# Kernel optimization log

Hardware: AMD Instinct MI355X
Metric: run time of the kernel (lower is better)

Reference implementation:

```python
import jax, jax.numpy as jnp
import numpy as np

LAMBDA = 1.0          # lambda_param
SIGMA = 1.0           # RBF bandwidth (sigkernel convention: exp(-||x-y||^2 / sigma))
DYADIC_ORDER = 2
F = 2 ** DYADIC_ORDER # dyadic refinement factor per time axis

B, M_POP, DIM, SEQ_LEN = 4, 16, 8, 65


def _rbf_gram(X, Y):
    # X: (m, L, d), Y: (n, L, d) -> static kernel Gram (m, n, L, L)
    sx = jnp.sum(X * X, -1)                       # (m, L)
    sy = jnp.sum(Y * Y, -1)                       # (n, L)
    inner = jnp.einsum('isd,jtd->ijst', X, Y)     # (m, n, L, L)
    d2 = sx[:, None, :, None] + sy[None, :, None, :] - 2.0 * inner
    return jnp.exp(-d2 / SIGMA)


def _increments(G):
    # double increment of the static Gram over time, then dyadic refinement
    inc = G[..., 1:, 1:] + G[..., :-1, :-1] - G[..., 1:, :-1] - G[..., :-1, 1:]
    inc = jnp.repeat(jnp.repeat(inc, F, axis=-2), F, axis=-1) / (F * F)
    return inc  # (..., S, S) with S = F*(L-1)


def _solve_pde(M):
    # Goursat PDE explicit finite-difference scheme (as in sigkernel):
    # K[i+1,j+1] = (K[i+1,j]+K[i,j+1])*(1 + m/2 + m^2/12) - K[i,j]*(1 - m^2/12)
    dtype = M.dtype
    S = M.shape[0]

    def row_step(prev_row, m_row):
        def cell(k_left, inp):
            k00, k01, m = inp
            a = 1.0 + 0.5 * m + m * m * (1.0 / 12.0)
            b = 1.0 - m * m * (1.0 / 12.0)
            k_new = (k_left + k01) * a - k00 * b
            return k_new, k_new
        _, tail = jax.lax.scan(cell, jnp.asarray(1.0, dtype),
                               (prev_row[:-1], prev_row[1:], m_row))
        new_row = jnp.concatenate([jnp.ones((1,), dtype), tail])
        return new_row, None

    row0 = jnp.ones((S + 1,), dtype)
    last_row, _ = jax.lax.scan(row_step, row0, M)
    return last_row[-1]


def _gram_sig(X, Y):
    # signature kernel Gram matrix: X (m,L,d), Y (n,L,d) -> (m,n)
    Minc = _increments(_rbf_gram(X, Y))
    return jax.vmap(jax.vmap(_solve_pde))(Minc)


def setup_inputs() -> dict:
    key = jax.random.key(0)
    k1, k2 = jax.random.split(key)
    generated_samples = jax.random.normal(k1, (B, M_POP, DIM, SEQ_LEN), dtype=jnp.float32)
    real_sample = jax.random.normal(k2, (B, DIM, SEQ_LEN), dtype=jnp.float32)
    return {"generated_samples": generated_samples, "real_sample": real_sample}


def reference(generated_samples, real_sample):
    # generated_samples: (B, m, dim, L); real_sample: (B, dim, L)
    gen = jnp.swapaxes(generated_samples, -1, -2)          # (B, m, L, d)
    real = jnp.swapaxes(real_sample, -1, -2)[:, None]      # (B, 1, L, d)
    m = gen.shape[1]
    K_XX = jax.vmap(_gram_sig)(gen, gen)                   # (B, m, m)
    K_XY = jax.vmap(_gram_sig)(gen, real)                  # (B, m, 1)
    self_sim = (jnp.sum(K_XX, axis=(-1, -2))
                - jnp.trace(K_XX, axis1=-2, axis2=-1)) / (m * (m - 1))
    cross_sim = jnp.mean(K_XY, axis=(-1, -2))
    return jnp.mean(LAMBDA / 2.0 * self_sim - cross_sim)
```

## Files before the change

kernel.cpp:

```cpp
#include <hip/hip_runtime.h>


#define SEQ   65
#define DIMS  8
#define MPOP  16
#define NBATCH 4
#define NPAIR_XX 120
#define NBLOCKS (NBATCH*(NPAIR_XX + MPOP))
#define MROW  194

__device__ __forceinline__ float wave_shr1(float x) {
    int xi = __builtin_bit_cast(int, x);
    int r  = __builtin_amdgcn_update_dpp(xi, xi, 0x138, 0xF, 0xF, false);
    return __builtin_bit_cast(float, r);
}
__device__ __forceinline__ float wave_shl1(float x) {
    int xi = __builtin_bit_cast(int, x);
    int r  = __builtin_amdgcn_update_dpp(xi, xi, 0x130, 0xF, 0xF, false);
    return __builtin_bit_cast(float, r);
}

__global__ __launch_bounds__(64, 1) void sigker_kernel(
    const float* __restrict__ gen,
    const float* __restrict__ realp,
    float* __restrict__ ws)
{
    __shared__ __align__(16) float YsF[SEQ * DIMS];
    __shared__ float R64[SEQ];
    __shared__ float YnL[SEQ];
    __shared__ __align__(16) float MmL[64 * MROW];

    const int tid = threadIdx.x;
    const int I   = tid;
    const bool lane0 = (I == 0);
    const int bid = blockIdx.x;

    {
        float4 z4 = make_float4(0.f, 0.f, 0.f, 0.f);
        float4* M4 = (float4*)MmL;
        #pragma unroll
        for (int k = 0; k < (64 * MROW) / 4 / 64; ++k)
            M4[k * 64 + tid] = z4;
        if (tid < 32) M4[48 * 64 + tid] = z4;
    }

    int b, ii, jj; bool cross;
    if (bid < NBATCH * NPAIR_XX) {
        b = bid / NPAIR_XX;
        int p = bid % NPAIR_XX;
        int i = 0, acc = 0;
        while (p >= acc + (MPOP - 1 - i)) { acc += (MPOP - 1 - i); ++i; }
        ii = i; jj = i + 1 + (p - acc); cross = false;
    } else {
        int t = bid - NBATCH * NPAIR_XX;
        b = t / MPOP; ii = t % MPOP; jj = 0; cross = true;
    }

    const float* Xg = gen + (size_t)(b * MPOP + ii) * (DIMS * SEQ);
    const float* Yg = cross ? (realp + (size_t)b * (DIMS * SEQ))
                            : (gen + (size_t)(b * MPOP + jj) * (DIMS * SEQ));

    for (int f = tid; f < SEQ * DIMS; f += 64) {
        int d = f / SEQ, s = f - d * SEQ;
        YsF[s * DIMS + d] = Yg[f];
    }
    float x0[DIMS], x64[DIMS];
    float xn0 = 0.f, xn64 = 0.f;
    #pragma unroll
    for (int d = 0; d < DIMS; ++d) {
        x0[d]  = Xg[d * SEQ + I];
        x64[d] = Xg[d * SEQ + 64];
        xn0  += x0[d]  * x0[d];
        xn64 += x64[d] * x64[d];
    }
    __syncthreads();

    for (int t = tid; t < SEQ; t += 64) {
        const float4* yv = (const float4*)&YsF[t * DIMS];
        float4 ya = yv[0], yb = yv[1];
        float yn  = ya.x*ya.x + ya.y*ya.y + ya.z*ya.z + ya.w*ya.w
                  + yb.x*yb.x + yb.y*yb.y + yb.z*yb.z + yb.w*yb.w;
        float dot = x64[0]*ya.x + x64[1]*ya.y + x64[2]*ya.z + x64[3]*ya.w
                  + x64[4]*yb.x + x64[5]*yb.y + x64[6]*yb.z + x64[7]*yb.w;
        YnL[t] = yn;
        R64[t] = __expf(2.f*dot - xn64 - yn);
    }
    __syncthreads();

    float* mrowW = &MmL[I * MROW + 64];
    float ep, enp;
    {
        const float4* yv = (const float4*)&YsF[0];
        float4 ya = yv[0], yb = yv[1];
        float dot = x0[0]*ya.x + x0[1]*ya.y + x0[2]*ya.z + x0[3]*ya.w
                  + x0[4]*yb.x + x0[5]*yb.y + x0[6]*yb.z + x0[7]*yb.w;
        float e  = __expf(2.f*dot - xn0 - YnL[0]);
        float en = wave_shl1(e);
        en = (I == 63) ? R64[0] : en;
        ep = e; enp = en;
    }
    #pragma unroll 4
    for (int t = 1; t < SEQ; ++t) {
        const float4* yv = (const float4*)&YsF[t * DIMS];
        float4 ya = yv[0], yb = yv[1];
        float dot = x0[0]*ya.x + x0[1]*ya.y + x0[2]*ya.z + x0[3]*ya.w
                  + x0[4]*yb.x + x0[5]*yb.y + x0[6]*yb.z + x0[7]*yb.w;
        float e  = __expf(2.f*dot - xn0 - YnL[t]);
        float en = wave_shl1(e);
        en = (I == 63) ? R64[t] : en;
        mrowW[t - 1] = ((en - enp) + (ep - e)) * (1.0f / 16.0f);
        ep = e; enp = en;
    }

    const float* mpde = &MmL[193 * I + 64];
    float l0 = 1.f, l1 = 1.f, l2 = 1.f, l3 = 1.f;
    float b0 = 1.f, b1 = 1.f, b2 = 1.f, b3 = 1.f;
    float cnext = 1.f;

#define STEP(MV) do {                                                   \
        float t0_ = wave_shr1(b0);                                      \
        float t1_ = wave_shr1(b1);                                      \
        float t2_ = wave_shr1(b2);                                      \
        float t3_ = wave_shr1(b3);                                      \
        if (lane0) { t0_ = 1.f; t1_ = 1.f; t2_ = 1.f; t3_ = 1.f; }      \
        float cc_ = cnext; cnext = t3_;                                 \
        float m_   = (MV);                                              \
        float q12_ = m_ * m_ * (1.0f / 12.0f);                          \
        float a_   = 1.0f + 0.5f * m_ + q12_;                           \
        float nb_  = q12_ - 1.0f;                                       \
        float u0_ = a_ * t0_ + nb_ * cc_;                               \
        float u1_ = a_ * t1_ + nb_ * t0_;                               \
        float u2_ = a_ * t2_ + nb_ * t1_;                               \
        float u3_ = a_ * t3_ + nb_ * t2_;                               \
        float q1_ = a_ * l0 + u0_;                                      \
        float q2_ = a_ * q1_ + u1_;                                     \
        float q3_ = a_ * q2_ + u2_;                                     \
        float q4_ = a_ * q3_ + u3_;                                     \
        u0_ = a_ * q1_ + nb_ * l0;  u1_ = a_ * q2_ + nb_ * q1_;         \
        u2_ = a_ * q3_ + nb_ * q2_; u3_ = a_ * q4_ + nb_ * q3_;         \
        float r1_ = a_ * l1 + u0_;                                      \
        float r2_ = a_ * r1_ + u1_;                                     \
        float r3_ = a_ * r2_ + u2_;                                     \
        float r4_ = a_ * r3_ + u3_;                                     \
        u0_ = a_ * r1_ + nb_ * l1;  u1_ = a_ * r2_ + nb_ * r1_;         \
        u2_ = a_ * r3_ + nb_ * r2_; u3_ = a_ * r4_ + nb_ * r3_;         \
        float s1_ = a_ * l2 + u0_;                                      \
        float s2_ = a_ * s1_ + u1_;                                     \
        float s3_ = a_ * s2_ + u2_;                                     \
        float s4_ = a_ * s3_ + u3_;                                     \
        u0_ = a_ * s1_ + nb_ * l2;  u1_ = a_ * s2_ + nb_ * s1_;         \
        u2_ = a_ * s3_ + nb_ * s2_; u3_ = a_ * s4_ + nb_ * s3_;         \
        float v1_ = a_ * l3 + u0_;                                      \
        float v2_ = a_ * v1_ + u1_;                                     \
        float v3_ = a_ * v2_ + u2_;                                     \
        float v4_ = a_ * v3_ + u3_;                                     \
        b0 = v1_; b1 = v2_; b2 = v3_; b3 = v4_;                         \
        l0 = q4_; l1 = r4_; l2 = s4_; l3 = v4_;                         \
    } while (0)

    float m0 = mpde[0], m1 = mpde[1], m2 = mpde[2], m3 = mpde[3];
    float m4 = mpde[4], m5 = mpde[5], m6 = mpde[6], m7 = mpde[7];

    for (int g = 0; g < 15; ++g) {
        const int nb_ = (g + 1) * 8;
        float n0 = mpde[nb_ + 0], n1 = mpde[nb_ + 1];
        float n2 = mpde[nb_ + 2], n3 = mpde[nb_ + 3];
        float n4 = mpde[nb_ + 4], n5 = mpde[nb_ + 5];
        float n6 = mpde[nb_ + 6], n7 = mpde[nb_ + 7];
        STEP(m0); STEP(m1); STEP(m2); STEP(m3);
        STEP(m4); STEP(m5); STEP(m6); STEP(m7);
        m0 = n0; m1 = n1; m2 = n2; m3 = n3;
        m4 = n4; m5 = n5; m6 = n6; m7 = n7;
    }
    STEP(m0); STEP(m1); STEP(m2); STEP(m3);
    STEP(m4); STEP(m5); STEP(m6);
#undef STEP

    if (tid == 63) {
        float w = cross ? (-1.0f / 32.0f) : (1.0f / 480.0f);
        ws[bid] = w * b3;
    }
}

__global__ __launch_bounds__(64, 1) void sigker_reduce(
    const float* __restrict__ ws, float* __restrict__ out)
{
    const int lane = threadIdx.x;
    float s = 0.f;
    for (int k = lane; k < NBLOCKS; k += 64) s += ws[k];
    #pragma unroll
    for (int off = 32; off >= 1; off >>= 1) s += __shfl_xor(s, off);
    if (lane == 0) out[0] = s;
}

extern "C" void kernel_launch(void* const* d_in, const int* in_sizes, int n_in,
                              void* d_out, int out_size, void* d_ws, size_t ws_size,
                              hipStream_t stream) {
    const float* gen   = (const float*)d_in[0];
    const float* realp = (const float*)d_in[1];
    if (n_in >= 2 && in_sizes[0] == NBATCH * DIMS * SEQ) {
        gen   = (const float*)d_in[1];
        realp = (const float*)d_in[0];
    }
    float* ws  = (float*)d_ws;
    float* out = (float*)d_out;
    sigker_kernel<<<NBLOCKS, 64, 0, stream>>>(gen, realp, ws);
    sigker_reduce<<<1, 64, 0, stream>>>(ws, out);
}
```

Baseline: 85.59 us.

## Fuse reduction via last-block atomic counter, shrink skewed LDS buffer, pack FMAs

Removes the separate reduction kernel by having the last block to finish (detected through an atomic counter and threadfence) sum the per-pair results. The launch now adds a memset for the counter. The skewed M buffer goes from a 194-stride zero-padded layout to a compact 66-stride row with clamped indexing, which drops the large LDS zero-fill and shrinks shared memory. The dot products and parts of the PDE update are rewritten with 2-wide float vectors to encourage packed FMA instructions.

New measurement: 91.72 us. 7.2% more time.

```diff
diff --git a/kernel.cpp b/kernel.cpp
--- a/kernel.cpp
+++ b/kernel.cpp
@@ -6,8 +6,11 @@
 #define MPOP  16
 #define NBATCH 4
 #define NPAIR_XX 120
-#define NBLOCKS (NBATCH*(NPAIR_XX + MPOP))
-#define MROW  194
+#define NPAIRS (NBATCH*(NPAIR_XX + MPOP))
+#define MST 66
+
+typedef float v2f __attribute__((ext_vector_type(2)));
+static __device__ __forceinline__ v2f mk2(float x, float y) { return (v2f){x, y}; }
 
 __device__ __forceinline__ float wave_shr1(float x) {
     int xi = __builtin_bit_cast(int, x);
@@ -19,30 +22,67 @@
     int r  = __builtin_amdgcn_update_dpp(xi, xi, 0x130, 0xF, 0xF, false);
     return __builtin_bit_cast(float, r);
 }
+__device__ __forceinline__ float ldm(const float* base, int idx) {
+    return base[idx < 0 ? 0 : idx];
+}
+
+struct PS { float l0,l1,l2,l3,b0,b1,b2,b3,cn; };
+
+__device__ __forceinline__ void pde_step(PS& s, float m, bool lane0) {
+    float t0 = wave_shr1(s.b0);  t0 = lane0 ? 1.f : t0;
+    float t1 = wave_shr1(s.b1);  t1 = lane0 ? 1.f : t1;
+    float t2 = wave_shr1(s.b2);  t2 = lane0 ? 1.f : t2;
+    float t3 = wave_shr1(s.b3);  t3 = lane0 ? 1.f : t3;
+    float c = s.cn; s.cn = t3;
+    float mm  = m * m;
+    float q12 = mm * (1.0f / 12.0f);
+    float a   = (1.0f + q12) + 0.5f * m;
+    float nb  = q12 - 1.0f;
+    v2f av = mk2(a, a), nv = mk2(nb, nb);
+    v2f u01 = av * mk2(t0, t1) + nv * mk2(c,  t0);
+    v2f u23 = av * mk2(t2, t3) + nv * mk2(t1, t2);
+    float q1 = a * s.l0 + u01.x;
+    float q2 = a * q1   + u01.y;
+    float q3 = a * q2   + u23.x;
+    float q4 = a * q3   + u23.y;
+    u01 = av * mk2(q1, q2) + nv * mk2(s.l0, q1);
+    u23 = av * mk2(q3, q4) + nv * mk2(q2,  q3);
+    float r1 = a * s.l1 + u01.x;
+    float r2 = a * r1   + u01.y;
+    float r3 = a * r2   + u23.x;
+    float r4 = a * r3   + u23.y;
+    u01 = av * mk2(r1, r2) + nv * mk2(s.l1, r1);
+    u23 = av * mk2(r3, r4) + nv * mk2(r2,  r3);
+    float w1 = a * s.l2 + u01.x;
+    float w2 = a * w1   + u01.y;
+    float w3 = a * w2   + u23.x;
+    float w4 = a * w3   + u23.y;
+    u01 = av * mk2(w1, w2) + nv * mk2(s.l2, w1);
+    u23 = av * mk2(w3, w4) + nv * mk2(w2,  w3);
+    float v1 = a * s.l3 + u01.x;
+    float v2 = a * v1   + u01.y;
+    float v3 = a * v2   + u23.x;
+    float v4 = a * v3   + u23.y;
+    s.b0=v1; s.b1=v2; s.b2=v3; s.b3=v4;
+    s.l0=q4; s.l1=r4; s.l2=w4; s.l3=v4;
+}
 
 __global__ __launch_bounds__(64, 1) void sigker_kernel(
     const float* __restrict__ gen,
     const float* __restrict__ realp,
-    float* __restrict__ ws)
+    float* __restrict__ ws,
+    unsigned* __restrict__ cnt,
+    float* __restrict__ out)
 {
     __shared__ __align__(16) float YsF[SEQ * DIMS];
+    __shared__ float YnL[SEQ];
     __shared__ float R64[SEQ];
-    __shared__ float YnL[SEQ];
-    __shared__ __align__(16) float MmL[64 * MROW];
+    __shared__ float MmL[64 * MST];
 
     const int tid = threadIdx.x;
     const int I   = tid;
     const bool lane0 = (I == 0);
     const int bid = blockIdx.x;
-
-    {
-        float4 z4 = make_float4(0.f, 0.f, 0.f, 0.f);
-        float4* M4 = (float4*)MmL;
-        #pragma unroll
-        for (int k = 0; k < (64 * MROW) / 4 / 64; ++k)
-            M4[k * 64 + tid] = z4;
-        if (tid < 32) M4[48 * 64 + tid] = z4;
-    }
 
     int b, ii, jj; bool cross;
     if (bid < NBATCH * NPAIR_XX) {
@@ -60,41 +100,54 @@
     const float* Yg = cross ? (realp + (size_t)b * (DIMS * SEQ))
                             : (gen + (size_t)(b * MPOP + jj) * (DIMS * SEQ));
 
+    MmL[MST * I] = 0.f;  MmL[MST * I + 65] = 0.f;
     for (int f = tid; f < SEQ * DIMS; f += 64) {
         int d = f / SEQ, s = f - d * SEQ;
         YsF[s * DIMS + d] = Yg[f];
     }
-    float x0[DIMS], x64[DIMS];
-    float xn0 = 0.f, xn64 = 0.f;
-    #pragma unroll
-    for (int d = 0; d < DIMS; ++d) {
-        x0[d]  = Xg[d * SEQ + I];
-        x64[d] = Xg[d * SEQ + 64];
-        xn0  += x0[d]  * x0[d];
-        xn64 += x64[d] * x64[d];
+    v2f x01, x23, x45, x67, z01, z23, z45, z67;
+    {
+        float xv[DIMS], zv[DIMS];
+        #pragma unroll
+        for (int d = 0; d < DIMS; ++d) {
+            xv[d] = Xg[d * SEQ + I];
+            zv[d] = Xg[d * SEQ + 64];
+        }
+        x01 = mk2(xv[0],xv[1]); x23 = mk2(xv[2],xv[3]);
+        x45 = mk2(xv[4],xv[5]); x67 = mk2(xv[6],xv[7]);
+        z01 = mk2(zv[0],zv[1]); z23 = mk2(zv[2],zv[3]);
+        z45 = mk2(zv[4],zv[5]); z67 = mk2(zv[6],zv[7]);
+    }
+    float xn0, xn64;
+    {
+        v2f sx = x01*x01 + x23*x23 + x45*x45 + x67*x67;
+        v2f sz = z01*z01 + z23*z23 + z45*z45 + z67*z67;
+        xn0 = sx.x + sx.y;  xn64 = sz.x + sz.y;
     }
     __syncthreads();
 
     for (int t = tid; t < SEQ; t += 64) {
         const float4* yv = (const float4*)&YsF[t * DIMS];
         float4 ya = yv[0], yb = yv[1];
-        float yn  = ya.x*ya.x + ya.y*ya.y + ya.z*ya.z + ya.w*ya.w
-                  + yb.x*yb.x + yb.y*yb.y + yb.z*yb.z + yb.w*yb.w;
-        float dot = x64[0]*ya.x + x64[1]*ya.y + x64[2]*ya.z + x64[3]*ya.w
-                  + x64[4]*yb.x + x64[5]*yb.y + x64[6]*yb.z + x64[7]*yb.w;
+        v2f y01 = mk2(ya.x,ya.y), y23 = mk2(ya.z,ya.w);
+        v2f y45 = mk2(yb.x,yb.y), y67 = mk2(yb.z,yb.w);
+        v2f sn = y01*y01 + y23*y23 + y45*y45 + y67*y67;
+        v2f sd = z01*y01 + z23*y23 + z45*y45 + z67*y67;
+        float yn  = sn.x + sn.y;
+        float dot = sd.x + sd.y;
         YnL[t] = yn;
         R64[t] = __expf(2.f*dot - xn64 - yn);
     }
     __syncthreads();
 
-    float* mrowW = &MmL[I * MROW + 64];
+    float* mrow = &MmL[MST * I];
     float ep, enp;
     {
         const float4* yv = (const float4*)&YsF[0];
         float4 ya = yv[0], yb = yv[1];
-        float dot = x0[0]*ya.x + x0[1]*ya.y + x0[2]*ya.z + x0[3]*ya.w
-                  + x0[4]*yb.x + x0[5]*yb.y + x0[6]*yb.z + x0[7]*yb.w;
-        float e  = __expf(2.f*dot - xn0 - YnL[0]);
+        v2f sd = x01*mk2(ya.x,ya.y) + x23*mk2(ya.z,ya.w)
+               + x45*mk2(yb.x,yb.y) + x67*mk2(yb.z,yb.w);
+        float e  = __expf(2.f*(sd.x + sd.y) - xn0 - YnL[0]);
         float en = wave_shl1(e);
         en = (I == 63) ? R64[0] : en;
         ep = e; enp = en;
@@ -103,94 +156,56 @@
     for (int t = 1; t < SEQ; ++t) {
         const float4* yv = (const float4*)&YsF[t * DIMS];
         float4 ya = yv[0], yb = yv[1];
-        float dot = x0[0]*ya.x + x0[1]*ya.y + x0[2]*ya.z + x0[3]*ya.w
-                  + x0[4]*yb.x + x0[5]*yb.y + x0[6]*yb.z + x0[7]*yb.w;
-        float e  = __expf(2.f*dot - xn0 - YnL[t]);
+        v2f sd = x01*mk2(ya.x,ya.y) + x23*mk2(ya.z,ya.w)
+               + x45*mk2(yb.x,yb.y) + x67*mk2(yb.z,yb.w);
+        float e  = __expf(2.f*(sd.x + sd.y) - xn0 - YnL[t]);
         float en = wave_shl1(e);
         en = (I == 63) ? R64[t] : en;
-        mrowW[t - 1] = ((en - enp) + (ep - e)) * (1.0f / 16.0f);
+        mrow[t] = ((en - enp) + (ep - e)) * (1.0f / 16.0f);
         ep = e; enp = en;
     }
 
-    const float* mpde = &MmL[193 * I + 64];
-    float l0 = 1.f, l1 = 1.f, l2 = 1.f, l3 = 1.f;
-    float b0 = 1.f, b1 = 1.f, b2 = 1.f, b3 = 1.f;
-    float cnext = 1.f;
-
-#define STEP(MV) do {                                                   \
-        float t0_ = wave_shr1(b0);                                      \
-        float t1_ = wave_shr1(b1);                                      \
-        float t2_ = wave_shr1(b2);                                      \
-        float t3_ = wave_shr1(b3);                                      \
-        if (lane0) { t0_ = 1.f; t1_ = 1.f; t2_ = 1.f; t3_ = 1.f; }      \
-        float cc_ = cnext; cnext = t3_;                                 \
-        float m_   = (MV);                                              \
-        float q12_ = m_ * m_ * (1.0f / 12.0f);                          \
-        float a_   = 1.0f + 0.5f * m_ + q12_;                           \
-        float nb_  = q12_ - 1.0f;                                       \
-        float u0_ = a_ * t0_ + nb_ * cc_;                               \
-        float u1_ = a_ * t1_ + nb_ * t0_;                               \
-        float u2_ = a_ * t2_ + nb_ * t1_;                               \
-        float u3_ = a_ * t3_ + nb_ * t2_;                               \
-        float q1_ = a_ * l0 + u0_;                                      \
-        float q2_ = a_ * q1_ + u1_;                                     \
-        float q3_ = a_ * q2_ + u2_;                                     \
-        float q4_ = a_ * q3_ + u3_;                                     \
-        u0_ = a_ * q1_ + nb_ * l0;  u1_ = a_ * q2_ + nb_ * q1_;         \
-        u2_ = a_ * q3_ + nb_ * q2_; u3_ = a_ * q4_ + nb_ * q3_;         \
-        float r1_ = a_ * l1 + u0_;                                      \
-        float r2_ = a_ * r1_ + u1_;                                     \
-        float r3_ = a_ * r2_ + u2_;                                     \
-        float r4_ = a_ * r3_ + u3_;                                     \
-        u0_ = a_ * r1_ + nb_ * l1;  u1_ = a_ * r2_ + nb_ * r1_;         \
-        u2_ = a_ * r3_ + nb_ * r2_; u3_ = a_ * r4_ + nb_ * r3_;         \
-        float s1_ = a_ * l2 + u0_;                                      \
-        float s2_ = a_ * s1_ + u1_;                                     \
-        float s3_ = a_ * s2_ + u2_;                                     \
-        float s4_ = a_ * s3_ + u3_;                                     \
-        u0_ = a_ * s1_ + nb_ * l2;  u1_ = a_ * s2_ + nb_ * s1_;         \
-        u2_ = a_ * s3_ + nb_ * s2_; u3_ = a_ * s4_ + nb_ * s3_;         \
-        float v1_ = a_ * l3 + u0_;                                      \
-        float v2_ = a_ * v1_ + u1_;                                     \
-        float v3_ = a_ * v2_ + u2_;                                     \
-        float v4_ = a_ * v3_ + u3_;                                     \
-        b0 = v1_; b1 = v2_; b2 = v3_; b3 = v4_;                         \
-        l0 = q4_; l1 = r4_; l2 = s4_; l3 = v4_;                         \
-    } while (0)
-
-    float m0 = mpde[0], m1 = mpde[1], m2 = mpde[2], m3 = mpde[3];
-    float m4 = mpde[4], m5 = mpde[5], m6 = mpde[6], m7 = mpde[7];
-
-    for (int g = 0; g < 15; ++g) {
-        const int nb_ = (g + 1) * 8;
-        float n0 = mpde[nb_ + 0], n1 = mpde[nb_ + 1];
-        float n2 = mpde[nb_ + 2], n3 = mpde[nb_ + 3];
-        float n4 = mpde[nb_ + 4], n5 = mpde[nb_ + 5];
-        float n6 = mpde[nb_ + 6], n7 = mpde[nb_ + 7];
-        STEP(m0); STEP(m1); STEP(m2); STEP(m3);
-        STEP(m4); STEP(m5); STEP(m6); STEP(m7);
-        m0 = n0; m1 = n1; m2 = n2; m3 = n3;
-        m4 = n4; m5 = n5; m6 = n6; m7 = n7;
-    }
-    STEP(m0); STEP(m1); STEP(m2); STEP(m3);
-    STEP(m4); STEP(m5); STEP(m6);
-#undef STEP
+    PS S = {1,1,1,1, 1,1,1,1, 1};
+    const int ib = 1 - I;
+    float m[8];
+    #pragma unroll
+    for (int k = 0; k < 8; ++k) m[k] = ldm(mrow, ib + k);
+
+    for (int g = 0; g < 14; ++g) {
+        float n[8];
+        const int D8 = g * 8 + 8;
+        #pragma unroll
+        for (int k = 0; k < 8; ++k) n[k] = ldm(mrow, ib + D8 + k);
+        #pragma unroll
+        for (int k = 0; k < 8; ++k) pde_step(S, m[k], lane0);
+        #pragma unroll
+        for (int k = 0; k < 8; ++k) m[k] = n[k];
+    }
+    float mt[7];
+    #pragma unroll
+    for (int k = 0; k < 7; ++k) mt[k] = ldm(mrow, ib + 120 + k);
+    #pragma unroll
+    for (int k = 0; k < 8; ++k) pde_step(S, m[k], lane0);
+    #pragma unroll
+    for (int k = 0; k < 7; ++k) pde_step(S, mt[k], lane0);
 
     if (tid == 63) {
         float w = cross ? (-1.0f / 32.0f) : (1.0f / 480.0f);
-        ws[bid] = w * b3;
-    }
-}
-
-__global__ __launch_bounds__(64, 1) void sigker_reduce(
-    const float* __restrict__ ws, float* __restrict__ out)
-{
-    const int lane = threadIdx.x;
-    float s = 0.f;
-    for (int k = lane; k < NBLOCKS; k += 64) s += ws[k];
-    #pragma unroll
-    for (int off = 32; off >= 1; off >>= 1) s += __shfl_xor(s, off);
-    if (lane == 0) out[0] = s;
+        ws[bid] = w * S.b3;
+    }
+
+    __threadfence();
+    unsigned old = 0;
+    if (tid == 0) old = atomicAdd(cnt, 1u);
+    old = __shfl(old, 0);
+    if (old == NPAIRS - 1) {
+        __threadfence();
+        float s = 0.f;
+        for (int k = tid; k < NPAIRS; k += 64) s += ws[k];
+        #pragma unroll
+        for (int off = 32; off >= 1; off >>= 1) s += __shfl_xor(s, off);
+        if (tid == 0) out[0] = s;
+    }
 }
 
 extern "C" void kernel_launch(void* const* d_in, const int* in_sizes, int n_in,
@@ -202,8 +217,9 @@
         gen   = (const float*)d_in[1];
         realp = (const float*)d_in[0];
     }
-    float* ws  = (float*)d_ws;
-    float* out = (float*)d_out;
-    sigker_kernel<<<NBLOCKS, 64, 0, stream>>>(gen, realp, ws);
-    sigker_reduce<<<1, 64, 0, stream>>>(ws, out);
-}
+    float*    ws  = (float*)d_ws;
+    unsigned* cnt = (unsigned*)((char*)d_ws + NPAIRS * sizeof(float));
+    float*    out = (float*)d_out;
+    hipMemsetAsync(cnt, 0, sizeof(unsigned), stream);
+    sigker_kernel<<<NPAIRS, 64, 0, stream>>>(gen, realp, ws, cnt, out);
+}
```
